# Kernel optimization log

Hardware: AMD Instinct MI355X
Metric: run time of the kernel (lower is better)

Reference implementation:

```python
import jax, jax.numpy as jnp
import numpy as np

SCALES = (1.0, 0.5, 0.25, 0.125)
POOLED_H, POOLED_W = 14, 14


def _convert_boxes(b):
    # bbox cols [0,1,3,4,6] -> (cx, cy, w, h, ry); lidar coords mapped to the
    # 200x176 BEV grid exactly as in convert_to_roi_list_format.
    cx = b[:, 0] * 175.0 / 70.4 + 0.5
    cy = (b[:, 1] + 40.0) * 199.0 / 80.0 + 0.5
    w = b[:, 3] * 175.0 / 70.4
    h = b[:, 4] * 199.0 / 80.0
    ang = b[:, 6]
    ids = jnp.zeros_like(cx)  # batch id hardcoded to 0, as in the torch code
    return jnp.stack([ids, cx, cy, w, h, ang], axis=1)  # [N,6]


def _bilinear(feat, y, x):
    # feat: [C,H,W]; y, x: [N,PH,PW] sample coordinates. ROIAlign semantics:
    # samples more than one pixel outside the map contribute zero; otherwise
    # clamp to the border and bilinearly interpolate.
    C, H, W = feat.shape
    valid = (y > -1.0) & (y < H) & (x > -1.0) & (x < W)
    y = jnp.clip(y, 0.0, H - 1)
    x = jnp.clip(x, 0.0, W - 1)
    y0 = jnp.floor(y).astype(jnp.int32)
    x0 = jnp.floor(x).astype(jnp.int32)
    y1 = jnp.minimum(y0 + 1, H - 1)
    x1 = jnp.minimum(x0 + 1, W - 1)
    ly = y - y0
    lx = x - x0
    hy = 1.0 - ly
    hx = 1.0 - lx
    v = (feat[:, y0, x0] * (hy * hx) + feat[:, y0, x1] * (hy * lx)
         + feat[:, y1, x0] * (ly * hx) + feat[:, y1, x1] * (ly * lx))  # [C,N,PH,PW]
    return jnp.where(valid, v, jnp.zeros_like(v))


def _rroi_align(feat, rois, scale):
    # feat: [C,H,W]; rois: [N,6] = (id, cx, cy, w, h, theta). One bilinear
    # sample at the center of each rotated output bin (RROIAlign affine map).
    cx = rois[:, 1] * scale
    cy = rois[:, 2] * scale
    rw = rois[:, 3] * scale
    rh = rois[:, 4] * scale
    th = rois[:, 5]
    # bin-center offsets in the box's local frame, in [-0.5, 0.5)
    fw = (jnp.arange(POOLED_W, dtype=feat.dtype) + 0.5) / POOLED_W - 0.5
    fh = (jnp.arange(POOLED_H, dtype=feat.dtype) + 0.5) / POOLED_H - 0.5
    lx = fw[None, None, :] * rw[:, None, None]  # [N,1,PW]
    ly = fh[None, :, None] * rh[:, None, None]  # [N,PH,1]
    c = jnp.cos(th)[:, None, None]
    s = jnp.sin(th)[:, None, None]
    x = cx[:, None, None] + lx * c - ly * s  # [N,PH,PW]
    y = cy[:, None, None] + lx * s + ly * c
    return jnp.transpose(_bilinear(feat, y, x), (1, 0, 2, 3))  # [N,C,PH,PW]


def setup_inputs() -> dict:
    key = jax.random.key(0)
    ks = jax.random.split(key, 8)
    d = {}
    shapes = [(1, 256, 200, 176), (1, 256, 100, 88), (1, 256, 50, 44), (1, 256, 25, 22)]
    for i, sh in enumerate(shapes):
        d[f"x{i}"] = jax.random.normal(ks[i], sh, dtype=jnp.float32)
    for i in range(4):
        u = jax.random.uniform(ks[4 + i], (512, 7), dtype=jnp.float32)
        bx = u[:, 0] * 60.0 + 5.0        # lidar x in [5, 65] m
        by = u[:, 1] * 70.0 - 35.0       # lidar y in [-35, 35] m
        bz = u[:, 2]
        bw = u[:, 3] * 2.0 + 1.5         # width ~ [1.5, 3.5] m
        bl = u[:, 4] * 4.0 + 3.0         # length ~ [3, 7] m
        bh = u[:, 5]
        ry = u[:, 6] * (2.0 * np.pi) - np.pi
        d[f"b{i}"] = jnp.stack([bx, by, bz, bw, bl, bh, ry], axis=1)
    return d


def reference(x0, x1, x2, x3, b0, b1, b2, b3):
    feats = (x0, x1, x2, x3)
    boxes = (b0, b1, b2, b3)
    outs = [_rroi_align(f[0], _convert_boxes(b), sc)
            for f, b, sc in zip(feats, boxes, SCALES)]
    return jnp.concatenate(outs, axis=0)  # [4*N, C, PH, PW]
```

## Files before the change

### kernel.cpp

```cpp
#include <hip/hip_runtime.h>

#define POOLED 14
#define NPOS   196
#define NQUAD  49
#define SF_CAP 9216
#define META_N 200

typedef float f4 __attribute__((ext_vector_type(4)));

__device__ __forceinline__ int swz(int s) { return s ^ ((s >> 3) & 7); }

__global__ __launch_bounds__(256)
void rroi_align_kernel(const float* __restrict__ f0, const float* __restrict__ f1,
                       const float* __restrict__ f2, const float* __restrict__ f3,
                       const float* __restrict__ b0, const float* __restrict__ b1,
                       const float* __restrict__ b2, const float* __restrict__ b3,
                       float* __restrict__ out)
{
    __shared__ float s_f[SF_CAP];
    __shared__ f4    s_meta[META_N];

    const int blk = blockIdx.x;
    const int level = blk >> 9;
    const int roi = blk & 511;
    const int tid = threadIdx.x;

    const float* feat; const float* box; int H; int W; float scale;
    switch (level) {
      case 0:  feat = f0; box = b0; H = 200; W = 176; scale = 1.0f;    break;
      case 1:  feat = f1; box = b1; H = 100; W = 88;  scale = 0.5f;    break;
      case 2:  feat = f2; box = b2; H = 50;  W = 44;  scale = 0.25f;   break;
      default: feat = f3; box = b3; H = 25;  W = 22;  scale = 0.125f;  break;
    }
    const int G     = 16 << level;
    const int NPASS = 16 >> level;
    const int HW    = H * W;

    const float* bp = box + roi * 7;
    const float cx  = (bp[0] * 175.0f / 70.4f + 0.5f) * scale;
    const float cy  = ((bp[1] + 40.0f) * 199.0f / 80.0f + 0.5f) * scale;
    const float rw  = (bp[3] * 175.0f / 70.4f) * scale;
    const float rh  = (bp[4] * 199.0f / 80.0f) * scale;
    const float cth = cosf(bp[6]), sth = sinf(bp[6]);

    const float ex = 0.5f * (fabsf(rw * cth) + fabsf(rh * sth));
    const float ey = 0.5f * (fabsf(rw * sth) + fabsf(rh * cth));
    const int Xlo = min(max((int)floorf(cx - ex), 0), W - 2);
    const int Xhi = min(W - 1, max((int)floorf(cx + ex) + 1, Xlo + 1));
    const int Ylo = min(max((int)floorf(cy - ey), 0), H - 1);
    const int Yhi = min(H - 1, max((int)floorf(cy + ey) + 1, Ylo + 1));
    const int bw = Xhi - Xlo + 1;
    const int bh = Yhi - Ylo + 1;
    const int SP = bw * bh;

    const unsigned M1 = (unsigned)(4294967296.0 / (double)SP) + 1u;
    const unsigned M2 = 262144u / (unsigned)bw + 1u;

    if (tid < NPOS) {
        const int ph = tid / POOLED;
        const int pw = tid - ph * POOLED;
        const float fwx = ((float)pw + 0.5f) / (float)POOLED - 0.5f;
        const float fhy = ((float)ph + 0.5f) / (float)POOLED - 0.5f;
        const float lx = fwx * rw;
        const float ly = fhy * rh;
        const float x = cx + lx * cth - ly * sth;
        const float y = cy + lx * sth + ly * cth;

        const bool valid = (y > -1.0f) & (y < (float)H) & (x > -1.0f) & (x < (float)W);
        const float yc = fminf(fmaxf(y, 0.0f), (float)(H - 1));
        const float xc = fminf(fmaxf(x, 0.0f), (float)(W - 1));
        const int y0 = (int)floorf(yc);
        const int x0 = (int)floorf(xc);
        const int y1 = min(y0 + 1, H - 1);
        const float dyw = yc - (float)y0;
        float dxw = xc - (float)x0;

        const float m = valid ? 1.0f : 0.0f;
        const float A = (1.0f - dyw) * m;
        const float B = dyw * m;

        int xb = x0;
        if (x0 == W - 1) { xb = W - 2; dxw = 1.0f; }

        const unsigned o0 = (unsigned)((y0 - Ylo) * bw + (xb - Xlo));
        const unsigned o1 = (unsigned)((y1 - Ylo) * bw + (xb - Xlo));
        const int slot = (tid & 3) * NQUAD + (tid >> 2);
        s_meta[swz(slot)] = (f4){dxw, A, B, __uint_as_float(o0 | (o1 << 16))};
    }

    float* const out_roi = out + (size_t)blk * (256 * NPOS);
    const int GITER = (G * NQUAD + 255) >> 8;

    for (int pass = 0; pass < NPASS; ++pass) {
        const int cbase = pass * G;
        const float* __restrict__ fpass = feat + (size_t)cbase * HW;

        const int E = G * SP;
        for (int el = tid; el < E; el += 256) {
            const int g   = (int)__umulhi((unsigned)el, M1);
            const int rem = el - g * SP;
            const int ry  = (int)(((unsigned)rem * M2) >> 18);
            const int rx  = rem - ry * bw;
            s_f[el] = fpass[g * HW + (Ylo + ry) * W + (Xlo + rx)];
        }
        __syncthreads();

        const int TMAX = G * NQUAD;
        #pragma unroll 1
        for (int it = 0; it < GITER; ++it) {
            const int t = it * 256 + tid;
            if (t < TMAX) {
                const int c = t / NQUAD;
                const int q = t - c * NQUAD;
                const float* __restrict__ fb = s_f + c * SP;
                f4 r;
                #pragma unroll
                for (int j = 0; j < 4; ++j) {
                    const f4 md = s_meta[swz(j * NQUAD + q)];
                    const float dxw = md.x, A = md.y, B = md.z;
                    const unsigned pk = __float_as_uint(md.w);
                    const int o0 = (int)(pk & 0xffffu);
                    const int o1 = (int)(pk >> 16);
                    const float hx = 1.0f - dxw;
                    const float t0 = fb[o0], t1 = fb[o0 + 1];
                    const float u0 = fb[o1], u1 = fb[o1 + 1];
                    r[j] = A * (t0 * hx + t1 * dxw) + B * (u0 * hx + u1 * dxw);
                }
                __builtin_nontemporal_store(r, (f4*)(out_roi + (size_t)4 * (cbase * NQUAD + t)));
            }
        }
        __syncthreads();
    }
}

extern "C" void kernel_launch(void* const* d_in, const int* in_sizes, int n_in,
                              void* d_out, int out_size, void* d_ws, size_t ws_size,
                              hipStream_t stream)
{
    const float* f0 = (const float*)d_in[0];
    const float* f1 = (const float*)d_in[1];
    const float* f2 = (const float*)d_in[2];
    const float* f3 = (const float*)d_in[3];
    const float* b0 = (const float*)d_in[4];
    const float* b1 = (const float*)d_in[5];
    const float* b2 = (const float*)d_in[6];
    const float* b3 = (const float*)d_in[7];
    float* out = (float*)d_out;

    rroi_align_kernel<<<2048, 256, 0, stream>>>(f0, f1, f2, f3, b0, b1, b2, b3, out);
}
```

Before: 540.0 us.

## Double-buffer feature staging with async global-to-LDS loads and register-held sample metadata

Replaces the synchronous gather-then-compute loop with a two-buffer pipeline in shared memory. The next channel group is loaded with global_load_lds (direct global-to-LDS DMA) while the current group is interpolated. Channel group size is now picked per ROI from its footprint, and bilinear metadata is kept in registers instead of LDS. The aim is to hide gather latency and raise occupancy (launch bounds 256,4, smaller LDS). In exchange there are more passes for large footprints, possible out-of-range staging reads clamped to E-1, and no explicit wait on the async LDS loads beyond __syncthreads.

Measured after the change: 491.5 us. 1.1x faster.

```diff
diff --git a/kernel.cpp b/kernel.cpp
--- a/kernel.cpp
+++ b/kernel.cpp
@@ -3,38 +3,34 @@
 #define POOLED 14
 #define NPOS   196
 #define NQUAD  49
-#define SF_CAP 9216
-#define META_N 200
+#define BUF_N  4096
 
 typedef float f4 __attribute__((ext_vector_type(4)));
+typedef __attribute__((address_space(1))) const unsigned int guint;
+typedef __attribute__((address_space(3))) unsigned int       luint;
 
-__device__ __forceinline__ int swz(int s) { return s ^ ((s >> 3) & 7); }
-
-__global__ __launch_bounds__(256)
+__global__ __launch_bounds__(256, 4)
 void rroi_align_kernel(const float* __restrict__ f0, const float* __restrict__ f1,
                        const float* __restrict__ f2, const float* __restrict__ f3,
                        const float* __restrict__ b0, const float* __restrict__ b1,
                        const float* __restrict__ b2, const float* __restrict__ b3,
                        float* __restrict__ out)
 {
-    __shared__ float s_f[SF_CAP];
-    __shared__ f4    s_meta[META_N];
+    __shared__ float s_f[2][BUF_N];
 
     const int blk = blockIdx.x;
     const int level = blk >> 9;
     const int roi = blk & 511;
     const int tid = threadIdx.x;
 
-    const float* feat; const float* box; int H; int W; float scale;
+    const float* feat; const float* box; int H, W; float scale;
     switch (level) {
       case 0:  feat = f0; box = b0; H = 200; W = 176; scale = 1.0f;    break;
       case 1:  feat = f1; box = b1; H = 100; W = 88;  scale = 0.5f;    break;
       case 2:  feat = f2; box = b2; H = 50;  W = 44;  scale = 0.25f;   break;
       default: feat = f3; box = b3; H = 25;  W = 22;  scale = 0.125f;  break;
     }
-    const int G     = 16 << level;
-    const int NPASS = 16 >> level;
-    const int HW    = H * W;
+    const int HW = H * W;
 
     const float* bp = box + roi * 7;
     const float cx  = (bp[0] * 175.0f / 70.4f + 0.5f) * scale;
@@ -53,12 +49,27 @@
     const int bh = Yhi - Ylo + 1;
     const int SP = bw * bh;
 
+    int Graw = BUF_N / SP;
+    int G = 1 << (31 - __clz(Graw));
+    if (G > 256) G = 256;
+    const int NPASS = 256 / G;
+    const int E     = G * SP;
+    const int KMAX  = (E + 255) >> 8;
+    const int GITER = (G + 4) / 5;
+
     const unsigned M1 = (unsigned)(4294967296.0 / (double)SP) + 1u;
     const unsigned M2 = 262144u / (unsigned)bw + 1u;
 
-    if (tid < NPOS) {
-        const int ph = tid / POOLED;
-        const int pw = tid - ph * POOLED;
+    const int q  = tid % NQUAD;
+    const int cg = tid / NQUAD;
+    const bool gok = (cg < 5);
+
+    f4 md[4];
+    #pragma unroll
+    for (int j = 0; j < 4; ++j) {
+        const int p  = q * 4 + j;
+        const int ph = p / POOLED;
+        const int pw = p - ph * POOLED;
         const float fwx = ((float)pw + 0.5f) / (float)POOLED - 0.5f;
         const float fhy = ((float)ph + 0.5f) / (float)POOLED - 0.5f;
         const float lx = fwx * rw;
@@ -84,52 +95,58 @@
 
         const unsigned o0 = (unsigned)((y0 - Ylo) * bw + (xb - Xlo));
         const unsigned o1 = (unsigned)((y1 - Ylo) * bw + (xb - Xlo));
-        const int slot = (tid & 3) * NQUAD + (tid >> 2);
-        s_meta[swz(slot)] = (f4){dxw, A, B, __uint_as_float(o0 | (o1 << 16))};
+        md[j] = (f4){dxw, A, B, __uint_as_float(o0 | (o1 << 16))};
     }
 
+    const int wbase = tid & 192;
+    const int lane  = tid & 63;
+
+    auto stage = [&](int pass, int bsel) {
+        const float* __restrict__ fp = feat + (size_t)(pass * G) * HW;
+        for (int j = 0; j < KMAX; ++j) {
+            int el = j * 256 + wbase + lane;
+            int els = min(el, E - 1);
+            int g   = (int)__umulhi((unsigned)els, M1);
+            int rem = els - g * SP;
+            int ry  = (int)(((unsigned)rem * M2) >> 18);
+            int rx  = rem - ry * bw;
+            const float* src = fp + g * HW + (Ylo + ry) * W + (Xlo + rx);
+            __builtin_amdgcn_global_load_lds((guint*)src,
+                (luint*)&s_f[bsel][j * 256 + wbase], 4, 0, 0);
+        }
+    };
+
     float* const out_roi = out + (size_t)blk * (256 * NPOS);
-    const int GITER = (G * NQUAD + 255) >> 8;
 
-    for (int pass = 0; pass < NPASS; ++pass) {
-        const int cbase = pass * G;
-        const float* __restrict__ fpass = feat + (size_t)cbase * HW;
+    stage(0, 0);
+    #pragma unroll 1
+    for (int k = 0; k < NPASS; ++k) {
+        __syncthreads();
+        if (k + 1 < NPASS) stage(k + 1, (k + 1) & 1);
 
-        const int E = G * SP;
-        for (int el = tid; el < E; el += 256) {
-            const int g   = (int)__umulhi((unsigned)el, M1);
-            const int rem = el - g * SP;
-            const int ry  = (int)(((unsigned)rem * M2) >> 18);
-            const int rx  = rem - ry * bw;
-            s_f[el] = fpass[g * HW + (Ylo + ry) * W + (Xlo + rx)];
-        }
-        __syncthreads();
-
-        const int TMAX = G * NQUAD;
+        const float* __restrict__ fbuf = s_f[k & 1];
+        const int cbase = k * G;
         #pragma unroll 1
         for (int it = 0; it < GITER; ++it) {
-            const int t = it * 256 + tid;
-            if (t < TMAX) {
-                const int c = t / NQUAD;
-                const int q = t - c * NQUAD;
-                const float* __restrict__ fb = s_f + c * SP;
+            const int c = cg + 5 * it;
+            if (gok && c < G) {
+                const float* __restrict__ fb = fbuf + c * SP;
                 f4 r;
                 #pragma unroll
                 for (int j = 0; j < 4; ++j) {
-                    const f4 md = s_meta[swz(j * NQUAD + q)];
-                    const float dxw = md.x, A = md.y, B = md.z;
-                    const unsigned pk = __float_as_uint(md.w);
+                    const f4 m = md[j];
+                    const unsigned pk = __float_as_uint(m.w);
                     const int o0 = (int)(pk & 0xffffu);
                     const int o1 = (int)(pk >> 16);
-                    const float hx = 1.0f - dxw;
+                    const float hx = 1.0f - m.x;
                     const float t0 = fb[o0], t1 = fb[o0 + 1];
                     const float u0 = fb[o1], u1 = fb[o1 + 1];
-                    r[j] = A * (t0 * hx + t1 * dxw) + B * (u0 * hx + u1 * dxw);
+                    r[j] = m.y * (t0 * hx + t1 * m.x) + m.z * (u0 * hx + u1 * m.x);
                 }
-                __builtin_nontemporal_store(r, (f4*)(out_roi + (size_t)4 * (cbase * NQUAD + t)));
+                __builtin_nontemporal_store(r,
+                    (f4*)(out_roi + (size_t)((cbase + c) * NPOS + 4 * q)));
             }
         }
-        __syncthreads();
     }
 }
 
```
